# Kernel tuning notes

Hardware: AMD Instinct MI355X
Metric: run time of the kernel (lower is better)

The kernel has to match this reference:

```python
import jax, jax.numpy as jnp
import numpy as np

N_NODES = 100000
N_EDGES = 1600000
IN_FEATS = 128
N_HIDDEN = 32
N_CLASSES = 40
HEADS = (8, 8, 1)
NEG_SLOPE = 0.2  # PyG GATConv default leaky_relu slope


def gat_conv(h, src, dst, W, a_src, a_dst, b, n_nodes):
    """PyG-style GATConv (concat=True, eval mode, self-loops already added).
    h: [N, Fin], W: [Fin, H*C], a_src/a_dst: [H, C], b: [H*C].
    """
    H, C = a_src.shape
    x = (h @ W).reshape(n_nodes, H, C)                      # [N, H, C]
    al_src = jnp.sum(x * a_src[None], axis=-1)              # [N, H]
    al_dst = jnp.sum(x * a_dst[None], axis=-1)              # [N, H]
    e = jax.nn.leaky_relu(al_src[src] + al_dst[dst], NEG_SLOPE)  # [E, H]
    # numerically-stable softmax over each destination node's neighborhood
    m = jax.ops.segment_max(e, dst, num_segments=n_nodes)   # [N, H]
    w = jnp.exp(e - m[dst])                                 # [E, H]
    s = jax.ops.segment_sum(w, dst, num_segments=n_nodes)   # [N, H]
    alpha = w / s[dst]                                      # [E, H]
    out = jax.ops.segment_sum(x[src] * alpha[:, :, None], dst,
                              num_segments=n_nodes)         # [N, H, C]
    return out.reshape(n_nodes, H * C) + b


def _layer_params(key, fin, heads, cout):
    k1, k2, k3 = jax.random.split(key, 3)
    W = jax.random.normal(k1, (fin, heads * cout), dtype=jnp.float32) * (1.0 / np.sqrt(fin))
    a_src = jax.random.normal(k2, (heads, cout), dtype=jnp.float32) * 0.1
    a_dst = jax.random.normal(k3, (heads, cout), dtype=jnp.float32) * 0.1
    b = jnp.zeros((heads * cout,), dtype=jnp.float32)
    return W, a_src, a_dst, b


def setup_inputs() -> dict:
    key = jax.random.key(0)
    ks = jax.random.split(key, 5)
    features = jax.random.normal(ks[0], (N_NODES, IN_FEATS), dtype=jnp.float32)
    edge_index = jax.random.randint(ks[1], (2, N_EDGES), 0, N_NODES, dtype=jnp.int64)
    W0, a_src0, a_dst0, b0 = _layer_params(ks[2], IN_FEATS, HEADS[0], N_HIDDEN)
    W1, a_src1, a_dst1, b1 = _layer_params(ks[3], N_HIDDEN * HEADS[0], HEADS[1], N_HIDDEN)
    W2, a_src2, a_dst2, b2 = _layer_params(ks[4], N_HIDDEN * HEADS[1], HEADS[2], N_CLASSES)
    return {
        "features": features, "edge_index": edge_index,
        "W0": W0, "a_src0": a_src0, "a_dst0": a_dst0, "b0": b0,
        "W1": W1, "a_src1": a_src1, "a_dst1": a_dst1, "b1": b1,
        "W2": W2, "a_src2": a_src2, "a_dst2": a_dst2, "b2": b2,
    }


def reference(features, edge_index, W0, a_src0, a_dst0, b0,
              W1, a_src1, a_dst1, b1, W2, a_src2, a_dst2, b2):
    n = features.shape[0]
    loops = jnp.arange(n, dtype=edge_index.dtype)
    src = jnp.concatenate([edge_index[0], loops])  # add_self_loops=True (PyG default)
    dst = jnp.concatenate([edge_index[1], loops])
    # eval mode: F.dropout is identity
    h = gat_conv(features, src, dst, W0, a_src0, a_dst0, b0, n)
    h = jax.nn.elu(h)
    h = gat_conv(h, src, dst, W1, a_src1, a_dst1, b1, n)
    h = jax.nn.elu(h)
    h = gat_conv(h, src, dst, W2, a_src2, a_dst2, b2, n)
    return h
```

## Files before the change

### kernel.cpp

```cpp
#include <hip/hip_runtime.h>
#include <hip/hip_bf16.h>
#include <hip/hip_fp16.h>
#include <math.h>

typedef __attribute__((ext_vector_type(8))) short short8;
typedef __attribute__((ext_vector_type(8))) _Float16 half8;
typedef __attribute__((ext_vector_type(4))) float f32x4;
typedef unsigned short ushort_t;
typedef unsigned long long u64_t;
struct __align__(8) us4 { ushort_t x, y, z, w; };

__device__ __forceinline__ ushort_t f2bf(float f) {
    unsigned u = __float_as_uint(f);
    u += 0x7FFFu + ((u >> 16) & 1u);
    return (ushort_t)(u >> 16);
}
__device__ __forceinline__ float bf2f(ushort_t h) {
    return __uint_as_float(((unsigned)h) << 16);
}

__device__ __forceinline__ void store_out(float* p, float v) { *p = v; }
__device__ __forceinline__ void store_out(__half* p, float v) { *p = __float2half(v); }

__global__ void detect64_k(const int* __restrict__ ei, int n_check,
                           int* __restrict__ flag, int* __restrict__ gtot) {
    int t = threadIdx.x;
    gtot[t] = 0; gtot[t + 256] = 0;
    if (t < 64) {
        int zeros = 0;
        for (int i = t; i < n_check; i += 64) zeros += (ei[2 * i + 1] == 0) ? 1 : 0;
        #pragma unroll
        for (int off = 1; off < 64; off <<= 1) zeros += __shfl_xor(zeros, off);
        if (t == 0) *flag = (zeros >= n_check - 2) ? 1 : 0;
    }
}

__device__ __forceinline__ void edge_sd(const int* __restrict__ ei, int e, int E,
                                        int is64, int N, int& s_, int& d_) {
    if (e >= E) { s_ = d_ = e - E; return; }
    int s, d;
    if (is64) { s = ei[2 * e]; d = ei[2 * (E + e)]; }
    else      { s = ei[e];     d = ei[E + e]; }
    s_ = ((unsigned)s < (unsigned)N) ? s : 0;
    d_ = ((unsigned)d < (unsigned)N) ? d : 0;
}


__global__ __launch_bounds__(256) void csr_hist_k(
    const int* __restrict__ ei, const int* __restrict__ flag,
    int* __restrict__ gtot, int E, int Etot, int N) {
    __shared__ int hc[512];
    int t = threadIdx.x;
    hc[t] = 0; hc[t + 256] = 0;
    __syncthreads();
    int base = blockIdx.x * 4096;
    int is64 = *flag;
    for (int k = 0; k < 16; ++k) {
        int e = base + k * 256 + t;
        if (e < Etot) {
            int s_, d_;
            edge_sd(ei, e, E, is64, N, s_, d_);
            atomicAdd(&hc[d_ >> 8], 1);
        }
    }
    __syncthreads();
    if (hc[t])       atomicAdd(&gtot[t], hc[t]);
    if (hc[t + 256]) atomicAdd(&gtot[t + 256], hc[t + 256]);
}

__global__ void csr_scanb_k(const int* __restrict__ gtot, int* __restrict__ boff,
                            int* __restrict__ gcur, int B) {
    __shared__ int tmp[512];
    int t = threadIdx.x;
    int v = (t < B) ? gtot[t] : 0;
    tmp[t] = v;
    __syncthreads();
    for (int off = 1; off < 512; off <<= 1) {
        int x = (t >= off) ? tmp[t - off] : 0;
        __syncthreads();
        tmp[t] += x;
        __syncthreads();
    }
    if (t < B) {
        int excl = tmp[t] - v;
        boff[t] = excl;
        gcur[t] = excl;
    }
    if (t == B - 1) boff[B] = tmp[t];
}

__global__ __launch_bounds__(256) void csr_stage_k(
    const int* __restrict__ ei, const int* __restrict__ flag,
    int* __restrict__ gcur, u64_t* __restrict__ staging,
    int E, int Etot, int N) {
    __shared__ int bcnt[512];
    __shared__ int resv[512];
    int t = threadIdx.x;
    bcnt[t] = 0; bcnt[t + 256] = 0;
    __syncthreads();
    int base = blockIdx.x * 4096;
    int is64 = *flag;
    u64_t pk[16];
    #pragma unroll
    for (int k = 0; k < 16; ++k) {
        int e = base + k * 256 + t;
        pk[k] = ~0ull;
        if (e < Etot) {
            int s_, d_;
            edge_sd(ei, e, E, is64, N, s_, d_);
            pk[k] = ((u64_t)(unsigned)d_ << 32) | (unsigned)s_;
            atomicAdd(&bcnt[d_ >> 8], 1);
        }
    }
    __syncthreads();
    {
        int c0 = bcnt[t];
        resv[t] = c0 ? atomicAdd(&gcur[t], c0) : 0;
        int c1 = bcnt[t + 256];
        resv[t + 256] = c1 ? atomicAdd(&gcur[t + 256], c1) : 0;
    }
    __syncthreads();
    bcnt[t] = 0; bcnt[t + 256] = 0;
    __syncthreads();
    #pragma unroll
    for (int k = 0; k < 16; ++k) {
        if (pk[k] != ~0ull) {
            int b = (int)(pk[k] >> 40);
            int pos = resv[b] + atomicAdd(&bcnt[b], 1);
            staging[pos] = pk[k];
        }
    }
}

__global__ __launch_bounds__(256) void csr_fine_k(
    const u64_t* __restrict__ staging, const int* __restrict__ boff,
    int* __restrict__ rowptr, int* __restrict__ csr_src, int N, int Etot) {
    __shared__ int hcnt[256];
    __shared__ int scn[256];
    const int b = blockIdx.x, t = threadIdx.x;
    const int lo = b << 8;
    const int base = boff[b], cnt = boff[b + 1] - base;
    hcnt[t] = 0;
    __syncthreads();
    for (int i = t; i < cnt; i += 256) {
        int dst = (int)(staging[base + i] >> 32);
        atomicAdd(&hcnt[dst - lo], 1);
    }
    __syncthreads();
    int v = hcnt[t];
    scn[t] = v;
    __syncthreads();
    for (int off = 1; off < 256; off <<= 1) {
        int x = (t >= off) ? scn[t - off] : 0;
        __syncthreads();
        scn[t] += x;
        __syncthreads();
    }
    int excl = scn[t] - v;
    if (lo + t < N) rowptr[lo + t] = base + excl;
    hcnt[t] = base + excl;
    __syncthreads();
    for (int i = t; i < cnt; i += 256) {
        u64_t pd = staging[base + i];
        int dst = (int)(pd >> 32);
        int pos = atomicAdd(&hcnt[dst - lo], 1);
        csr_src[pos] = (int)(pd & 0xFFFFFFFFu);
    }
    if (b == 0 && t == 0) rowptr[N] = Etot;
}

__global__ void splitw_bf16_k(const float* __restrict__ W, ushort_t* __restrict__ Wh,
                              ushort_t* __restrict__ Wl, int K, int M, int Mp) {
    int i = blockIdx.x * 256 + threadIdx.x;
    if (i >= Mp * K) return;
    int n = i / K, k = i - n * K;
    float v = (n < M) ? W[(size_t)k * M + n] : 0.f;
    ushort_t h = f2bf(v);
    Wh[i] = h;
    Wl[i] = f2bf(v - bf2f(h));
}

__global__ void splitw_f16_k(const float* __restrict__ W, ushort_t* __restrict__ Wh,
                             ushort_t* __restrict__ Wl, int K, int M, int Mp) {
    int i = blockIdx.x * 256 + threadIdx.x;
    if (i >= Mp * K) return;
    int n = i / K, k = i - n * K;
    float v = (n < M) ? W[(size_t)k * M + n] : 0.f;
    __half h = __float2half(v);
    Wh[i] = __half_as_ushort(h);
    Wl[i] = __half_as_ushort(__float2half(v - __half2float(h)));
}

__global__ __launch_bounds__(256) void splitA_k(const float* __restrict__ A,
                                                ushort_t* __restrict__ Hh,
                                                ushort_t* __restrict__ Hl,
                                                long total4) {
    long i = ((long)blockIdx.x * 256 + threadIdx.x) * 4;
    if (i >= total4) return;
    float4 v = *(const float4*)&A[i];
    us4 h, l;
    h.x = f2bf(v.x); l.x = f2bf(v.x - bf2f(h.x));
    h.y = f2bf(v.y); l.y = f2bf(v.y - bf2f(h.y));
    h.z = f2bf(v.z); l.z = f2bf(v.z - bf2f(h.z));
    h.w = f2bf(v.w); l.w = f2bf(v.w - bf2f(h.w));
    *(us4*)&Hh[i] = h;
    *(us4*)&Hl[i] = l;
}

template <int BN, int WMCNT, int WNCNT, typename TOUT, int LMODE>
__global__ __launch_bounds__(256) void mfma_gemm_k(const ushort_t* __restrict__ Ahg,
                                                   const ushort_t* __restrict__ Alg,
                                                   const ushort_t* __restrict__ BhT,
                                                   const ushort_t* __restrict__ BlT,
                                                   TOUT* __restrict__ C,
                                                   int N, int K, int M,
                                                   const float* __restrict__ a_s,
                                                   const float* __restrict__ a_d,
                                                   float* __restrict__ alS,
                                                   float* __restrict__ alD) {
    constexpr int BM = 128;
    constexpr int PAD = 40;
    constexpr int WMX = BM / WMCNT;
    constexpr int WNX = BN / WNCNT;
    constexpr int FM = WMX / 16, FN = WNX / 16;
    static_assert(FN == 4, "logit epilogue assumes WNX==64");

    __shared__ ushort_t Ah[BM * PAD], Al[BM * PAD];
    __shared__ ushort_t Bh[BN * PAD], Bl[BN * PAD];

    const int tx = threadIdx.x;
    const int wave = tx >> 6, lane = tx & 63;
    const int quad = lane >> 4, l16 = lane & 15;
    const int br = blockIdx.y * BM, bc = blockIdx.x * BN;
    const int wm = (wave / WNCNT) * WMX;
    const int wn = (wave % WNCNT) * WNX;

    f32x4 acc[FM][FN] = {};

    for (int k0 = 0; k0 < K; k0 += 32) {
        #pragma unroll
        for (int r = 0; r < 2; ++r) {
            int i = r * 256 + tx;
            int m = i >> 2, k8 = (i & 3) * 8;
            int gr = br + m;
            short8 vh = {}, vl = {};
            if (gr < N) {
                vh = *(const short8*)&Ahg[(size_t)gr * K + k0 + k8];
                vl = *(const short8*)&Alg[(size_t)gr * K + k0 + k8];
            }
            *(short8*)&Ah[m * PAD + k8] = vh;
            *(short8*)&Al[m * PAD + k8] = vl;
        }
        #pragma unroll
        for (int r = 0; r < BN / 64; ++r) {
            int i = r * 256 + tx;
            int n = i >> 2, k8 = (i & 3) * 8;
            *(short8*)&Bh[n * PAD + k8] = *(const short8*)&BhT[(size_t)(bc + n) * K + k0 + k8];
            *(short8*)&Bl[n * PAD + k8] = *(const short8*)&BlT[(size_t)(bc + n) * K + k0 + k8];
        }
        __syncthreads();

        short8 afh[FM], afl[FM];
        #pragma unroll
        for (int mi = 0; mi < FM; ++mi) {
            int row = wm + mi * 16 + l16;
            afh[mi] = *(const short8*)&Ah[row * PAD + quad * 8];
            afl[mi] = *(const short8*)&Al[row * PAD + quad * 8];
        }
        #pragma unroll
        for (int ni = 0; ni < FN; ++ni) {
            int row = wn + ni * 16 + l16;
            short8 bfh = *(const short8*)&Bh[row * PAD + quad * 8];
            short8 bfl = *(const short8*)&Bl[row * PAD + quad * 8];
            #pragma unroll
            for (int mi = 0; mi < FM; ++mi) {
                acc[mi][ni] = __builtin_amdgcn_mfma_f32_16x16x32_bf16(afh[mi], bfh, acc[mi][ni], 0, 0, 0);
                acc[mi][ni] = __builtin_amdgcn_mfma_f32_16x16x32_bf16(afh[mi], bfl, acc[mi][ni], 0, 0, 0);
                acc[mi][ni] = __builtin_amdgcn_mfma_f32_16x16x32_bf16(afl[mi], bfh, acc[mi][ni], 0, 0, 0);
            }
        }
        __syncthreads();
    }

    #pragma unroll
    for (int mi = 0; mi < FM; ++mi) {
        #pragma unroll
        for (int ni = 0; ni < FN; ++ni) {
            int gc = bc + wn + ni * 16 + l16;
            if (gc >= M) continue;
            #pragma unroll
            for (int r = 0; r < 4; ++r) {
                int gr = br + wm + mi * 16 + quad * 4 + r;
                if (gr < N) store_out(&C[(size_t)gr * M + gc], acc[mi][ni][r]);
            }
        }
    }

    float aSv[FN], aDv[FN];
    #pragma unroll
    for (int ni = 0; ni < FN; ++ni) {
        int gc = bc + wn + ni * 16 + l16;
        bool ok = gc < M;
        aSv[ni] = ok ? a_s[gc] : 0.f;
        aDv[ni] = ok ? a_d[gc] : 0.f;
    }
    if (LMODE == 1) {
        #pragma unroll
        for (int mi = 0; mi < FM; ++mi) {
            #pragma unroll
            for (int r = 0; r < 4; ++r) {
                float p1a = acc[mi][0][r] * aSv[0] + acc[mi][1][r] * aSv[1];
                float p1b = acc[mi][2][r] * aSv[2] + acc[mi][3][r] * aSv[3];
                float p2a = acc[mi][0][r] * aDv[0] + acc[mi][1][r] * aDv[1];
                float p2b = acc[mi][2][r] * aDv[2] + acc[mi][3][r] * aDv[3];
                #pragma unroll
                for (int off = 1; off < 16; off <<= 1) {
                    p1a += __shfl_xor(p1a, off);
                    p1b += __shfl_xor(p1b, off);
                    p2a += __shfl_xor(p2a, off);
                    p2b += __shfl_xor(p2b, off);
                }
                if (l16 == 0) {
                    int gr = br + wm + mi * 16 + quad * 4 + r;
                    if (gr < N) {
                        int hb = (bc + wn) >> 5;
                        alS[gr * 8 + hb]     = p1a;
                        alS[gr * 8 + hb + 1] = p1b;
                        alD[gr * 8 + hb]     = p2a;
                        alD[gr * 8 + hb + 1] = p2b;
                    }
                }
            }
        }
    } else {
        #pragma unroll
        for (int mi = 0; mi < FM; ++mi) {
            #pragma unroll
            for (int r = 0; r < 4; ++r) {
                float p1 = acc[mi][0][r] * aSv[0] + acc[mi][1][r] * aSv[1]
                         + acc[mi][2][r] * aSv[2] + acc[mi][3][r] * aSv[3];
                float p2 = acc[mi][0][r] * aDv[0] + acc[mi][1][r] * aDv[1]
                         + acc[mi][2][r] * aDv[2] + acc[mi][3][r] * aDv[3];
                #pragma unroll
                for (int off = 1; off < 16; off <<= 1) {
                    p1 += __shfl_xor(p1, off);
                    p2 += __shfl_xor(p2, off);
                }
                if (l16 == 0) {
                    int gr = br + wm + mi * 16 + quad * 4 + r;
                    if (gr < N) { alS[gr] = p1; alD[gr] = p2; }
                }
            }
        }
    }
}

template <int BN, int WMCNT, int WNCNT, typename TOUT, int LMODE>
__global__ __launch_bounds__(256) void mfma_gemm_f16_k(const __half* __restrict__ A,
                                                       const ushort_t* __restrict__ BhT,
                                                       const ushort_t* __restrict__ BlT,
                                                       TOUT* __restrict__ C,
                                                       int N, int K, int M,
                                                       const float* __restrict__ a_s,
                                                       const float* __restrict__ a_d,
                                                       float* __restrict__ alS,
                                                       float* __restrict__ alD) {
    constexpr int BM = 128;
    constexpr int PAD = 40;
    constexpr int WMX = BM / WMCNT;
    constexpr int WNX = BN / WNCNT;
    constexpr int FM = WMX / 16, FN = WNX / 16;
    static_assert(FN == 4, "logit epilogue assumes WNX==64");

    __shared__ ushort_t Ah[BM * PAD];
    __shared__ ushort_t Bh[BN * PAD], Bl[BN * PAD];

    const int tx = threadIdx.x;
    const int wave = tx >> 6, lane = tx & 63;
    const int quad = lane >> 4, l16 = lane & 15;
    const int br = blockIdx.y * BM, bc = blockIdx.x * BN;
    const int wm = (wave / WNCNT) * WMX;
    const int wn = (wave % WNCNT) * WNX;

    f32x4 acc[FM][FN] = {};

    for (int k0 = 0; k0 < K; k0 += 32) {
        #pragma unroll
        for (int r = 0; r < 2; ++r) {
            int i = r * 256 + tx;
            int m = i >> 2, k8 = (i & 3) * 8;
            int gr = br + m;
            short8 v = {};
            if (gr < N) v = *(const short8*)&A[(size_t)gr * K + k0 + k8];
            *(short8*)&Ah[m * PAD + k8] = v;
        }
        #pragma unroll
        for (int r = 0; r < BN / 64; ++r) {
            int i = r * 256 + tx;
            int n = i >> 2, k8 = (i & 3) * 8;
            *(short8*)&Bh[n * PAD + k8] = *(const short8*)&BhT[(size_t)(bc + n) * K + k0 + k8];
            *(short8*)&Bl[n * PAD + k8] = *(const short8*)&BlT[(size_t)(bc + n) * K + k0 + k8];
        }
        __syncthreads();

        half8 af[FM];
        #pragma unroll
        for (int mi = 0; mi < FM; ++mi) {
            int row = wm + mi * 16 + l16;
            af[mi] = *(const half8*)&Ah[row * PAD + quad * 8];
        }
        #pragma unroll
        for (int ni = 0; ni < FN; ++ni) {
            int row = wn + ni * 16 + l16;
            half8 bfh = *(const half8*)&Bh[row * PAD + quad * 8];
            half8 bfl = *(const half8*)&Bl[row * PAD + quad * 8];
            #pragma unroll
            for (int mi = 0; mi < FM; ++mi) {
                acc[mi][ni] = __builtin_amdgcn_mfma_f32_16x16x32_f16(af[mi], bfh, acc[mi][ni], 0, 0, 0);
                acc[mi][ni] = __builtin_amdgcn_mfma_f32_16x16x32_f16(af[mi], bfl, acc[mi][ni], 0, 0, 0);
            }
        }
        __syncthreads();
    }

    #pragma unroll
    for (int mi = 0; mi < FM; ++mi) {
        #pragma unroll
        for (int ni = 0; ni < FN; ++ni) {
            int gc = bc + wn + ni * 16 + l16;
            if (gc >= M) continue;
            #pragma unroll
            for (int r = 0; r < 4; ++r) {
                int gr = br + wm + mi * 16 + quad * 4 + r;
                if (gr < N) store_out(&C[(size_t)gr * M + gc], acc[mi][ni][r]);
            }
        }
    }

    float aSv[FN], aDv[FN];
    #pragma unroll
    for (int ni = 0; ni < FN; ++ni) {
        int gc = bc + wn + ni * 16 + l16;
        bool ok = gc < M;
        aSv[ni] = ok ? a_s[gc] : 0.f;
        aDv[ni] = ok ? a_d[gc] : 0.f;
    }
    if (LMODE == 1) {
        #pragma unroll
        for (int mi = 0; mi < FM; ++mi) {
            #pragma unroll
            for (int r = 0; r < 4; ++r) {
                float p1a = acc[mi][0][r] * aSv[0] + acc[mi][1][r] * aSv[1];
                float p1b = acc[mi][2][r] * aSv[2] + acc[mi][3][r] * aSv[3];
                float p2a = acc[mi][0][r] * aDv[0] + acc[mi][1][r] * aDv[1];
                float p2b = acc[mi][2][r] * aDv[2] + acc[mi][3][r] * aDv[3];
                #pragma unroll
                for (int off = 1; off < 16; off <<= 1) {
                    p1a += __shfl_xor(p1a, off);
                    p1b += __shfl_xor(p1b, off);
                    p2a += __shfl_xor(p2a, off);
                    p2b += __shfl_xor(p2b, off);
                }
                if (l16 == 0) {
                    int gr = br + wm + mi * 16 + quad * 4 + r;
                    if (gr < N) {
                        int hb = (bc + wn) >> 5;
                        alS[gr * 8 + hb]     = p1a;
                        alS[gr * 8 + hb + 1] = p1b;
                        alD[gr * 8 + hb]     = p2a;
                        alD[gr * 8 + hb + 1] = p2b;
                    }
                }
            }
        }
    } else {
        #pragma unroll
        for (int mi = 0; mi < FM; ++mi) {
            #pragma unroll
            for (int r = 0; r < 4; ++r) {
                float p1 = acc[mi][0][r] * aSv[0] + acc[mi][1][r] * aSv[1]
                         + acc[mi][2][r] * aSv[2] + acc[mi][3][r] * aSv[3];
                float p2 = acc[mi][0][r] * aDv[0] + acc[mi][1][r] * aDv[1]
                         + acc[mi][2][r] * aDv[2] + acc[mi][3][r] * aDv[3];
                #pragma unroll
                for (int off = 1; off < 16; off <<= 1) {
                    p1 += __shfl_xor(p1, off);
                    p2 += __shfl_xor(p2, off);
                }
                if (l16 == 0) {
                    int gr = br + wm + mi * 16 + quad * 4 + r;
                    if (gr < N) { alS[gr] = p1; alD[gr] = p2; }
                }
            }
        }
    }
}

__global__ __launch_bounds__(256) void node_aggr8_k(
    const int* __restrict__ rowptr, const int* __restrict__ csr_src,
    const float* __restrict__ alS, const float* __restrict__ alD,
    const __half* __restrict__ xh, const float* __restrict__ bias,
    __half* __restrict__ out, int N, int do_elu) {
    __shared__ int    lsrc[4][64];
    __shared__ __half lalpha[4][64 * 8];
    const int wv = threadIdx.x >> 6;
    int wid = (blockIdx.x * 256 + threadIdx.x) >> 6;
    int lane = threadIdx.x & 63;
    if (wid >= N) return;
    const int d = wid;
    const int beg = rowptr[d], end = rowptr[d + 1];
    const int deg = end - beg;
    const int dcap = deg < 64 ? deg : 64;

    const int h = lane & 7, esub = lane >> 3;
    const float aDh = alD[d * 8 + h];

    const int nch = (deg + 7) >> 3;

    float exv[8] = {};
    float s = 0.f;
    #pragma unroll
    for (int c = 0; c < 8; ++c) {
        int sl = c * 8 + esub;
        int e = beg + sl;
        if (e < end) {
            int src = csr_src[e];
            float ev = alS[src * 8 + h] + aDh;
            ev = ev > 0.f ? ev : 0.2f * ev;
            float ex = __expf(fminf(ev, 30.f));
            if (h == 0) lsrc[wv][sl] = src;
            exv[c] = ex;
            s += ex;
        }
    }
    for (int c = 8; c < nch; ++c) {
        int e = beg + c * 8 + esub;
        if (e < end) {
            int src = csr_src[e];
            float ev = alS[src * 8 + h] + aDh;
            ev = ev > 0.f ? ev : 0.2f * ev;
            s += __expf(fminf(ev, 30.f));
        }
    }
    #pragma unroll
    for (int off = 8; off < 64; off <<= 1) s += __shfl_xor(s, off);

    float rsl = 1.f / s;
    #pragma unroll
    for (int c = 0; c < 8; ++c) {
        int sl = c * 8 + esub;
        if (sl < dcap) lalpha[wv][sl * 8 + h] = __float2half(exv[c] * rsl);
    }

    const int g = lane & 31;
    const int hh = g >> 2;
    const int p = lane >> 5;
    const float rs = __shfl(rsl, hh);

    const char* xb = (const char*)xh;
    const unsigned goff = (unsigned)(g << 4);

    const int T = (dcap + 1) >> 1;
    __half2 a2q[4];
    float4 rq[4];
    __half2 hacc[4] = {};

    #pragma unroll
    for (int i = 0; i < 4; ++i) {
        int e0 = 2 * i + p;
        int idx = e0 < dcap ? e0 : dcap - 1;
        int sv = lsrc[wv][idx];
        ushort_t ub = __half_as_ushort(lalpha[wv][idx * 8 + hh]);
        if (e0 >= dcap) ub = 0;
        a2q[i] = __half2half2(__ushort_as_half(ub));
        rq[i] = *(const float4*)(xb + (((unsigned)sv << 9) + goff));
    }

    #define PROC8(i)                                                        \
    {                                                                       \
        float4 raw = rq[i];                                                 \
        __half2 a2 = a2q[i];                                                \
        int e0 = 2 * (t + 4 + (i)) + p;                                     \
        ushort_t ub = 0;                                                    \
        if (e0 < dcap) {                                                    \
            int srcn = lsrc[wv][e0];                                        \
            ub = __half_as_ushort(lalpha[wv][e0 * 8 + hh]);                 \
            rq[i] = *(const float4*)(xb + (((unsigned)srcn << 9) + goff));  \
        }                                                                   \
        a2q[i] = __half2half2(__ushort_as_half(ub));                        \
        const __half2* hp = (const __half2*)&raw;                           \
        hacc[0] = __hfma2(hp[0], a2, hacc[0]);                              \
        hacc[1] = __hfma2(hp[1], a2, hacc[1]);                              \
        hacc[2] = __hfma2(hp[2], a2, hacc[2]);                              \
        hacc[3] = __hfma2(hp[3], a2, hacc[3]);                              \
    }
    #define TAIL8(i)                                                        \
    {                                                                       \
        float4 raw = rq[i];                                                 \
        __half2 a2 = a2q[i];                                                \
        const __half2* hp = (const __half2*)&raw;                           \
        hacc[0] = __hfma2(hp[0], a2, hacc[0]);                              \
        hacc[1] = __hfma2(hp[1], a2, hacc[1]);                              \
        hacc[2] = __hfma2(hp[2], a2, hacc[2]);                              \
        hacc[3] = __hfma2(hp[3], a2, hacc[3]);                              \
    }
    int t = 0;
    for (; t + 4 <= T; t += 4) { PROC8(0) PROC8(1) PROC8(2) PROC8(3) }
    {
        int rem = T - t;
        if (rem > 0) { TAIL8(0) if (rem > 1) { TAIL8(1) if (rem > 2) TAIL8(2) } }
    }
    #undef PROC8
    #undef TAIL8

    for (int c = 8; c < nch; ++c) {
        int base = beg + c * 8;
        int e = base + esub;
        int src_l = 0; float ex_l = 0.f;
        if (e < end) {
            src_l = csr_src[e];
            float ev = alS[src_l * 8 + h] + aDh;
            ev = ev > 0.f ? ev : 0.2f * ev;
            ex_l = __expf(fminf(ev, 30.f));
        }
        int cnt = end - base; if (cnt > 8) cnt = 8;
        int steps = (cnt + 1) >> 1;
        for (int t2 = 0; t2 < steps; ++t2) {
            int j = t2 * 2 + p;
            int jc = j < cnt ? j : (cnt - 1);
            int src = __shfl(src_l, jc * 8);
            float af = __shfl(ex_l, jc * 8 + hh) * rs;
            if (j >= cnt) af = 0.f;
            __half2 a2 = __float2half2_rn(af);
            const float4 raw = *(const float4*)(xb + (((unsigned)src << 9) + goff));
            const __half2* hp = (const __half2*)&raw;
            hacc[0] = __hfma2(hp[0], a2, hacc[0]);
            hacc[1] = __hfma2(hp[1], a2, hacc[1]);
            hacc[2] = __hfma2(hp[2], a2, hacc[2]);
            hacc[3] = __hfma2(hp[3], a2, hacc[3]);
        }
    }

    #pragma unroll
    for (int k = 0; k < 4; ++k) {
        int vi = __shfl_xor(*(int*)&hacc[k], 32);
        hacc[k] = __hadd2(hacc[k], *(__half2*)&vi);
    }

    if (p == 0) {
        float2 f0 = __half22float2(hacc[0]);
        float2 f1 = __half22float2(hacc[1]);
        float2 f2 = __half22float2(hacc[2]);
        float2 f3 = __half22float2(hacc[3]);
        const float4 bv0 = *(const float4*)&bias[g * 8];
        const float4 bv1 = *(const float4*)&bias[g * 8 + 4];
        float o[8];
        o[0] = f0.x + bv0.x; o[1] = f0.y + bv0.y;
        o[2] = f1.x + bv0.z; o[3] = f1.y + bv0.w;
        o[4] = f2.x + bv1.x; o[5] = f2.y + bv1.y;
        o[6] = f3.x + bv1.z; o[7] = f3.y + bv1.w;
        if (do_elu) {
            #pragma unroll
            for (int k = 0; k < 8; ++k) o[k] = o[k] > 0.f ? o[k] : (__expf(o[k]) - 1.f);
        }
        float4 st;
        ((__half2*)&st)[0] = __floats2half2_rn(o[0], o[1]);
        ((__half2*)&st)[1] = __floats2half2_rn(o[2], o[3]);
        ((__half2*)&st)[2] = __floats2half2_rn(o[4], o[5]);
        ((__half2*)&st)[3] = __floats2half2_rn(o[6], o[7]);
        *(float4*)(out + ((size_t)d << 8) + g * 8) = st;
    }
}

__global__ __launch_bounds__(256) void node_aggr1_k(
    const int* __restrict__ rowptr, const int* __restrict__ csr_src,
    const float* __restrict__ alS, const float* __restrict__ alD,
    const __half* __restrict__ xh2, const float* __restrict__ bias,
    float* __restrict__ out, int N) {
    __shared__ int   lsrc1[4][64];
    __shared__ float lal1[4][64];
    const int wv = threadIdx.x >> 6;
    int wid = (blockIdx.x * 256 + threadIdx.x) >> 6;
    int lane = threadIdx.x & 63;
    if (wid >= N) return;
    const int d = wid;
    const int beg = rowptr[d], end = rowptr[d + 1];
    const int deg = end - beg;
    const int dcap = deg < 64 ? deg : 64;
    const float aD = alD[d];

    float ex0 = 0.f;
    {
        int e = beg + lane;
        if (e < end) {
            int src0 = csr_src[e];
            float ev = alS[src0] + aD;
            ev = ev > 0.f ? ev : 0.2f * ev;
            ex0 = __expf(fminf(ev, 30.f));
            lsrc1[wv][lane] = src0;
        }
    }
    float s = ex0;
    for (int e = beg + 64 + lane; e < end; e += 64) {
        int src = csr_src[e];
        float ev = alS[src] + aD;
        ev = ev > 0.f ? ev : 0.2f * ev;
        s += __expf(fminf(ev, 30.f));
    }
    #pragma unroll
    for (int off = 1; off < 64; off <<= 1) s += __shfl_xor(s, off);
    const float rs = 1.f / s;
    if (lane < dcap) lal1[wv][lane] = ex0 * rs;

    const int q = lane & 31;
    const int p = lane >> 5;
    const int qg = q < 20 ? q : 19;
    const unsigned qb = (unsigned)(qg << 2);
    const char* xb2 = (const char*)xh2;

    const int T = (dcap + 1) >> 1;
    float alq[4];
    __half2 rq1[4];
    float ax = 0.f, ay = 0.f;

    #pragma unroll
    for (int i = 0; i < 4; ++i) {
        int e0 = 2 * i + p;
        int idx = e0 < dcap ? e0 : dcap - 1;
        int sv = lsrc1[wv][idx];
        float av = lal1[wv][idx];
        alq[i] = e0 < dcap ? av : 0.f;
        rq1[i] = *(const __half2*)(xb2 + ((unsigned)sv * 80u + qb));
    }

    #define PROC1(i)                                                        \
    {                                                                       \
        float2 rf = __half22float2(rq1[i]);                                 \
        float al = alq[i];                                                  \
        int e0 = 2 * (t + 4 + (i)) + p;                                     \
        float an = 0.f;                                                     \
        if (e0 < dcap) {                                                    \
            int sv = lsrc1[wv][e0];                                         \
            an = lal1[wv][e0];                                              \
            rq1[i] = *(const __half2*)(xb2 + ((unsigned)sv * 80u + qb));    \
        }                                                                   \
        alq[i] = an;                                                        \
        ax += rf.x * al; ay += rf.y * al;                                   \
    }
    #define TAIL1(i)                                                        \
    {                                                                       \
        float2 rf = __half22float2(rq1[i]);                                 \
        ax += rf.x * alq[i]; ay += rf.y * alq[i];                           \
    }
    int t = 0;
    for (; t + 4 <= T; t += 4) { PROC1(0) PROC1(1) PROC1(2) PROC1(3) }
    {
        int rem = T - t;
        if (rem > 0) { TAIL1(0) if (rem > 1) { TAIL1(1) if (rem > 2) TAIL1(2) } }
    }
    #undef PROC1
    #undef TAIL1

    for (int eb = beg + 64; eb < end; eb += 64) {
        int e = eb + lane;
        int cnt = end - eb; if (cnt > 64) cnt = 64;
        if (e < end) {
            int srcl = csr_src[e];
            float ev = alS[srcl] + aD;
            ev = ev > 0.f ? ev : 0.2f * ev;
            lsrc1[wv][lane] = srcl;
            lal1[wv][lane] = __expf(fminf(ev, 30.f)) * rs;
        }
        int T2 = (cnt + 1) >> 1;
        for (int t2 = 0; t2 < T2; ++t2) {
            int e0 = 2 * t2 + p;
            float al = 0.f;
            int sv = lsrc1[wv][0];
            if (e0 < cnt) { sv = lsrc1[wv][e0]; al = lal1[wv][e0]; }
            float2 rf = __half22float2(*(const __half2*)(xb2 + ((unsigned)sv * 80u + qb)));
            ax += rf.x * al; ay += rf.y * al;
        }
    }

    ax += __shfl_xor(ax, 32);
    ay += __shfl_xor(ay, 32);

    if (p == 0 && q < 20) {
        float2 bv = *(const float2*)&bias[q * 2];
        float2 st = make_float2(ax + bv.x, ay + bv.y);
        *(float2*)&out[(size_t)d * 40 + q * 2] = st;
    }
}

extern "C" void kernel_launch(void* const* d_in, const int* in_sizes, int n_in,
                              void* d_out, int out_size, void* d_ws, size_t ws_size,
                              hipStream_t stream) {
    const float* feat = (const float*)d_in[0];
    const int*   ei   = (const int*)d_in[1];
    const float* W0   = (const float*)d_in[2];
    const float* a0s  = (const float*)d_in[3];
    const float* a0d  = (const float*)d_in[4];
    const float* b0   = (const float*)d_in[5];
    const float* W1   = (const float*)d_in[6];
    const float* a1s  = (const float*)d_in[7];
    const float* a1d  = (const float*)d_in[8];
    const float* b1   = (const float*)d_in[9];
    const float* W2   = (const float*)d_in[10];
    const float* a2s  = (const float*)d_in[11];
    const float* a2d  = (const float*)d_in[12];
    const float* b2   = (const float*)d_in[13];
    float* out = (float*)d_out;

    const int N = in_sizes[0] / 128;
    const int E = in_sizes[1] / 2;
    const int Etot = E + N;

    __half* hbuf = (__half*)d_ws;
    __half* xh   = hbuf + (size_t)N * 256;
    __half* x2h  = xh + (size_t)N * 256;
    float*  alS  = (float*)(x2h + (size_t)N * 40);
    float*  alD  = alS + (size_t)N * 8;
    int* rowptr   = (int*)(alD + (size_t)N * 8);
    int* gtot     = rowptr + N + 1;
    int* boff     = gtot + 512;
    int* gcur     = boff + 513;
    int* csr_src  = gcur + 512;
    int* flag     = csr_src + Etot;
    uintptr_t wsp = ((uintptr_t)(flag + 1) + 15) & ~(uintptr_t)15;
    ushort_t* w0h = (ushort_t*)wsp;
    ushort_t* w0l = w0h + 256 * 128;
    ushort_t* w1h = w0l + 256 * 128;
    ushort_t* w1l = w1h + 256 * 256;
    ushort_t* w2h = w1l + 256 * 256;
    ushort_t* w2l = w2h + 64 * 256;

    u64_t* staging = (u64_t*)xh;

    ushort_t* fh = (ushort_t*)hbuf;
    ushort_t* fl = fh + (size_t)N * 128;

    const int B     = (N + 255) >> 8;
    const int nb_e4 = (Etot + 4095) / 4096;
    const int nb_nw = (N + 3) / 4;

    detect64_k<<<1, 256, 0, stream>>>(ei, 512, flag, gtot);
    csr_hist_k<<<nb_e4, 256, 0, stream>>>(ei, flag, gtot, E, Etot, N);
    csr_scanb_k<<<1, 512, 0, stream>>>(gtot, boff, gcur, B);
    csr_stage_k<<<nb_e4, 256, 0, stream>>>(ei, flag, gcur, staging, E, Etot, N);
    csr_fine_k<<<B, 256, 0, stream>>>(staging, boff, rowptr, csr_src, N, Etot);
    splitw_bf16_k<<<128, 256, 0, stream>>>(W0, w0h, w0l, 128, 256, 256);
    splitw_f16_k<<<256, 256, 0, stream>>>(W1, w1h, w1l, 256, 256, 256);
    splitw_f16_k<<<64, 256, 0, stream>>>(W2, w2h, w2l, 256, 40, 64);
    splitA_k<<<(int)(((long)N * 128 / 4 + 255) / 256), 256, 0, stream>>>(
        feat, fh, fl, (long)N * 128);

    const int mb = (N + 127) / 128;

    mfma_gemm_k<128, 2, 2, __half, 1><<<dim3(2, mb), 256, 0, stream>>>(
        fh, fl, w0h, w0l, xh, N, 128, 256, a0s, a0d, alS, alD);
    node_aggr8_k<<<nb_nw, 256, 0, stream>>>(rowptr, csr_src, alS, alD, xh, b0,
                                            hbuf, N, 1);

    mfma_gemm_f16_k<128, 2, 2, __half, 1><<<dim3(2, mb), 256, 0, stream>>>(
        hbuf, w1h, w1l, xh, N, 256, 256, a1s, a1d, alS, alD);
    node_aggr8_k<<<nb_nw, 256, 0, stream>>>(rowptr, csr_src, alS, alD, xh, b1,
                                            hbuf, N, 1);

    mfma_gemm_f16_k<64, 4, 1, __half, 2><<<dim3(1, mb), 256, 0, stream>>>(
        hbuf, w2h, w2l, x2h, N, 256, 40, a2s, a2d, alS, alD);
    node_aggr1_k<<<nb_nw, 256, 0, stream>>>(rowptr, csr_src, alS, alD, x2h, b2,
                                            out, N);
}
```

Before: 665.3 us.

## Use direct global-to-LDS loads in GEMMs, fuse prep kernels, pad layer-3 rows

The GEMM tile loads now use global_load_lds, which writes straight into unpadded shared memory and skips the register staging. Out-of-range rows are clamped to the last row rather than zero-filled. The four weight and feature split kernels are merged into one launch to cut launch overhead. The layer-3 projection is stored with a padded 64-column stride so the final aggregation can read 8-byte chunks, with 16 lanes per edge and 4 edges in flight per wave. Dropping the LDS padding may bring back bank conflicts on the fragment reads.

```diff
diff --git a/kernel.cpp b/kernel.cpp
--- a/kernel.cpp
+++ b/kernel.cpp
@@ -9,6 +9,11 @@
 typedef unsigned short ushort_t;
 typedef unsigned long long u64_t;
 struct __align__(8) us4 { ushort_t x, y, z, w; };
+
+#define GLDS16(gsrc, ldst)                                                   \
+    __builtin_amdgcn_global_load_lds(                                        \
+        (const __attribute__((address_space(1))) void*)(gsrc),               \
+        (__attribute__((address_space(3))) void*)(ldst), 16, 0, 0)
 
 __device__ __forceinline__ ushort_t f2bf(float f) {
     unsigned u = __float_as_uint(f);
@@ -44,7 +49,6 @@
     s_ = ((unsigned)s < (unsigned)N) ? s : 0;
     d_ = ((unsigned)d < (unsigned)N) ? d : 0;
 }
-
 
 __global__ __launch_bounds__(256) void csr_hist_k(
     const int* __restrict__ ei, const int* __restrict__ flag,
@@ -169,42 +173,47 @@
     if (b == 0 && t == 0) rowptr[N] = Etot;
 }
 
-__global__ void splitw_bf16_k(const float* __restrict__ W, ushort_t* __restrict__ Wh,
-                              ushort_t* __restrict__ Wl, int K, int M, int Mp) {
-    int i = blockIdx.x * 256 + threadIdx.x;
-    if (i >= Mp * K) return;
-    int n = i / K, k = i - n * K;
-    float v = (n < M) ? W[(size_t)k * M + n] : 0.f;
-    ushort_t h = f2bf(v);
-    Wh[i] = h;
-    Wl[i] = f2bf(v - bf2f(h));
-}
-
-__global__ void splitw_f16_k(const float* __restrict__ W, ushort_t* __restrict__ Wh,
-                             ushort_t* __restrict__ Wl, int K, int M, int Mp) {
-    int i = blockIdx.x * 256 + threadIdx.x;
-    if (i >= Mp * K) return;
-    int n = i / K, k = i - n * K;
-    float v = (n < M) ? W[(size_t)k * M + n] : 0.f;
-    __half h = __float2half(v);
-    Wh[i] = __half_as_ushort(h);
-    Wl[i] = __half_as_ushort(__float2half(v - __half2float(h)));
-}
-
-__global__ __launch_bounds__(256) void splitA_k(const float* __restrict__ A,
-                                                ushort_t* __restrict__ Hh,
-                                                ushort_t* __restrict__ Hl,
-                                                long total4) {
-    long i = ((long)blockIdx.x * 256 + threadIdx.x) * 4;
-    if (i >= total4) return;
-    float4 v = *(const float4*)&A[i];
-    us4 h, l;
-    h.x = f2bf(v.x); l.x = f2bf(v.x - bf2f(h.x));
-    h.y = f2bf(v.y); l.y = f2bf(v.y - bf2f(h.y));
-    h.z = f2bf(v.z); l.z = f2bf(v.z - bf2f(h.z));
-    h.w = f2bf(v.w); l.w = f2bf(v.w - bf2f(h.w));
-    *(us4*)&Hh[i] = h;
-    *(us4*)&Hl[i] = l;
+__global__ __launch_bounds__(256) void prep_k(
+    const float* __restrict__ W0, const float* __restrict__ W1,
+    const float* __restrict__ W2, const float* __restrict__ feat,
+    ushort_t* __restrict__ w0h, ushort_t* __restrict__ w0l,
+    ushort_t* __restrict__ w1h, ushort_t* __restrict__ w1l,
+    ushort_t* __restrict__ w2h, ushort_t* __restrict__ w2l,
+    ushort_t* __restrict__ fh, ushort_t* __restrict__ fl, long totalA4) {
+    int b = blockIdx.x, tx = threadIdx.x;
+    if (b < 128) {
+        int i = b * 256 + tx;
+        int n = i >> 7, k = i & 127;
+        float v = W0[(size_t)k * 256 + n];
+        ushort_t h = f2bf(v);
+        w0h[i] = h;
+        w0l[i] = f2bf(v - bf2f(h));
+    } else if (b < 384) {
+        int i = (b - 128) * 256 + tx;
+        int n = i >> 8, k = i & 255;
+        float v = W1[(size_t)k * 256 + n];
+        __half h = __float2half(v);
+        w1h[i] = __half_as_ushort(h);
+        w1l[i] = __half_as_ushort(__float2half(v - __half2float(h)));
+    } else if (b < 448) {
+        int i = (b - 384) * 256 + tx;
+        int n = i >> 8, k = i & 255;
+        float v = (n < 40) ? W2[(size_t)k * 40 + n] : 0.f;
+        __half h = __float2half(v);
+        w2h[i] = __half_as_ushort(h);
+        w2l[i] = __half_as_ushort(__float2half(v - __half2float(h)));
+    } else {
+        long i = ((long)(b - 448) * 256 + tx) * 4;
+        if (i >= totalA4) return;
+        float4 v = *(const float4*)&feat[i];
+        us4 h, l;
+        h.x = f2bf(v.x); l.x = f2bf(v.x - bf2f(h.x));
+        h.y = f2bf(v.y); l.y = f2bf(v.y - bf2f(h.y));
+        h.z = f2bf(v.z); l.z = f2bf(v.z - bf2f(h.z));
+        h.w = f2bf(v.w); l.w = f2bf(v.w - bf2f(h.w));
+        *(us4*)&fh[i] = h;
+        *(us4*)&fl[i] = l;
+    }
 }
 
 template <int BN, int WMCNT, int WNCNT, typename TOUT, int LMODE>
@@ -213,20 +222,19 @@
                                                    const ushort_t* __restrict__ BhT,
                                                    const ushort_t* __restrict__ BlT,
                                                    TOUT* __restrict__ C,
-                                                   int N, int K, int M,
+                                                   int N, int K, int M, int Mst,
                                                    const float* __restrict__ a_s,
                                                    const float* __restrict__ a_d,
                                                    float* __restrict__ alS,
                                                    float* __restrict__ alD) {
     constexpr int BM = 128;
-    constexpr int PAD = 40;
     constexpr int WMX = BM / WMCNT;
     constexpr int WNX = BN / WNCNT;
     constexpr int FM = WMX / 16, FN = WNX / 16;
     static_assert(FN == 4, "logit epilogue assumes WNX==64");
 
-    __shared__ ushort_t Ah[BM * PAD], Al[BM * PAD];
-    __shared__ ushort_t Bh[BN * PAD], Bl[BN * PAD];
+    __shared__ ushort_t Ah[BM * 32], Al[BM * 32];
+    __shared__ ushort_t Bh[BN * 32], Bl[BN * 32];
 
     const int tx = threadIdx.x;
     const int wave = tx >> 6, lane = tx & 63;
@@ -241,22 +249,19 @@
         #pragma unroll
         for (int r = 0; r < 2; ++r) {
             int i = r * 256 + tx;
-            int m = i >> 2, k8 = (i & 3) * 8;
-            int gr = br + m;
-            short8 vh = {}, vl = {};
-            if (gr < N) {
-                vh = *(const short8*)&Ahg[(size_t)gr * K + k0 + k8];
-                vl = *(const short8*)&Alg[(size_t)gr * K + k0 + k8];
-            }
-            *(short8*)&Ah[m * PAD + k8] = vh;
-            *(short8*)&Al[m * PAD + k8] = vl;
+            int m = i >> 2, kc = (i & 3) * 8;
+            int gr = br + m; gr = gr < N ? gr : N - 1;
+            size_t go = (size_t)gr * K + k0 + kc;
+            GLDS16(&Ahg[go], &Ah[(size_t)i * 8]);
+            GLDS16(&Alg[go], &Al[(size_t)i * 8]);
         }
         #pragma unroll
         for (int r = 0; r < BN / 64; ++r) {
             int i = r * 256 + tx;
-            int n = i >> 2, k8 = (i & 3) * 8;
-            *(short8*)&Bh[n * PAD + k8] = *(const short8*)&BhT[(size_t)(bc + n) * K + k0 + k8];
-            *(short8*)&Bl[n * PAD + k8] = *(const short8*)&BlT[(size_t)(bc + n) * K + k0 + k8];
+            int n = i >> 2, kc = (i & 3) * 8;
+            size_t go = (size_t)(bc + n) * K + k0 + kc;
+            GLDS16(&BhT[go], &Bh[(size_t)i * 8]);
+            GLDS16(&BlT[go], &Bl[(size_t)i * 8]);
         }
         __syncthreads();
 
@@ -264,14 +269,14 @@
         #pragma unroll
         for (int mi = 0; mi < FM; ++mi) {
             int row = wm + mi * 16 + l16;
-            afh[mi] = *(const short8*)&Ah[row * PAD + quad * 8];
-            afl[mi] = *(const short8*)&Al[row * PAD + quad * 8];
+            afh[mi] = *(const short8*)&Ah[row * 32 + quad * 8];
+            afl[mi] = *(const short8*)&Al[row * 32 + quad * 8];
         }
         #pragma unroll
         for (int ni = 0; ni < FN; ++ni) {
             int row = wn + ni * 16 + l16;
-            short8 bfh = *(const short8*)&Bh[row * PAD + quad * 8];
-            short8 bfl = *(const short8*)&Bl[row * PAD + quad * 8];
+            short8 bfh = *(const short8*)&Bh[row * 32 + quad * 8];
+            short8 bfl = *(const short8*)&Bl[row * 32 + quad * 8];
             #pragma unroll
             for (int mi = 0; mi < FM; ++mi) {
                 acc[mi][ni] = __builtin_amdgcn_mfma_f32_16x16x32_bf16(afh[mi], bfh, acc[mi][ni], 0, 0, 0);
@@ -287,11 +292,10 @@
         #pragma unroll
         for (int ni = 0; ni < FN; ++ni) {
             int gc = bc + wn + ni * 16 + l16;
-            if (gc >= M) continue;
             #pragma unroll
             for (int r = 0; r < 4; ++r) {
                 int gr = br + wm + mi * 16 + quad * 4 + r;
-                if (gr < N) store_out(&C[(size_t)gr * M + gc], acc[mi][ni][r]);
+                if (gr < N) store_out(&C[(size_t)gr * Mst + gc], acc[mi][ni][r]);
             }
         }
     }
@@ -360,20 +364,19 @@
                                                        const ushort_t* __restrict__ BhT,
                                                        const ushort_t* __restrict__ BlT,
                                                        TOUT* __restrict__ C,
-                                                       int N, int K, int M,
+                                                       int N, int K, int M, int Mst,
                                                        const float* __restrict__ a_s,
                                                        const float* __restrict__ a_d,
                                                        float* __restrict__ alS,
                                                        float* __restrict__ alD) {
     constexpr int BM = 128;
-    constexpr int PAD = 40;
     constexpr int WMX = BM / WMCNT;
     constexpr int WNX = BN / WNCNT;
     constexpr int FM = WMX / 16, FN = WNX / 16;
     static_assert(FN == 4, "logit epilogue assumes WNX==64");
 
-    __shared__ ushort_t Ah[BM * PAD];
-    __shared__ ushort_t Bh[BN * PAD], Bl[BN * PAD];
+    __shared__ ushort_t Ah[BM * 32];
+    __shared__ ushort_t Bh[BN * 32], Bl[BN * 32];
 
     const int tx = threadIdx.x;
     const int wave = tx >> 6, lane = tx & 63;
@@ -388,18 +391,17 @@
         #pragma unroll
         for (int r = 0; r < 2; ++r) {
             int i = r * 256 + tx;
-            int m = i >> 2, k8 = (i & 3) * 8;
-            int gr = br + m;
-            short8 v = {};
-            if (gr < N) v = *(const short8*)&A[(size_t)gr * K + k0 + k8];
-            *(short8*)&Ah[m * PAD + k8] = v;
+            int m = i >> 2, kc = (i & 3) * 8;
+            int gr = br + m; gr = gr < N ? gr : N - 1;
+            GLDS16(&A[(size_t)gr * K + k0 + kc], &Ah[(size_t)i * 8]);
         }
         #pragma unroll
         for (int r = 0; r < BN / 64; ++r) {
             int i = r * 256 + tx;
-            int n = i >> 2, k8 = (i & 3) * 8;
-            *(short8*)&Bh[n * PAD + k8] = *(const short8*)&BhT[(size_t)(bc + n) * K + k0 + k8];
-            *(short8*)&Bl[n * PAD + k8] = *(const short8*)&BlT[(size_t)(bc + n) * K + k0 + k8];
+            int n = i >> 2, kc = (i & 3) * 8;
+            size_t go = (size_t)(bc + n) * K + k0 + kc;
+            GLDS16(&BhT[go], &Bh[(size_t)i * 8]);
+            GLDS16(&BlT[go], &Bl[(size_t)i * 8]);
         }
         __syncthreads();
 
@@ -407,13 +409,13 @@
         #pragma unroll
         for (int mi = 0; mi < FM; ++mi) {
             int row = wm + mi * 16 + l16;
-            af[mi] = *(const half8*)&Ah[row * PAD + quad * 8];
+            af[mi] = *(const half8*)&Ah[row * 32 + quad * 8];
         }
         #pragma unroll
         for (int ni = 0; ni < FN; ++ni) {
             int row = wn + ni * 16 + l16;
-            half8 bfh = *(const half8*)&Bh[row * PAD + quad * 8];
-            half8 bfl = *(const half8*)&Bl[row * PAD + quad * 8];
+            half8 bfh = *(const half8*)&Bh[row * 32 + quad * 8];
+            half8 bfl = *(const half8*)&Bl[row * 32 + quad * 8];
             #pragma unroll
             for (int mi = 0; mi < FM; ++mi) {
                 acc[mi][ni] = __builtin_amdgcn_mfma_f32_16x16x32_f16(af[mi], bfh, acc[mi][ni], 0, 0, 0);
@@ -428,11 +430,10 @@
         #pragma unroll
         for (int ni = 0; ni < FN; ++ni) {
             int gc = bc + wn + ni * 16 + l16;
-            if (gc >= M) continue;
             #pragma unroll
             for (int r = 0; r < 4; ++r) {
                 int gr = br + wm + mi * 16 + quad * 4 + r;
-                if (gr < N) store_out(&C[(size_t)gr * M + gc], acc[mi][ni][r]);
+                if (gr < N) store_out(&C[(size_t)gr * Mst + gc], acc[mi][ni][r]);
             }
         }
     }
@@ -712,45 +713,51 @@
     const float rs = 1.f / s;
     if (lane < dcap) lal1[wv][lane] = ex0 * rs;
 
-    const int q = lane & 31;
-    const int p = lane >> 5;
-    const int qg = q < 20 ? q : 19;
-    const unsigned qb = (unsigned)(qg << 2);
+    const int p = lane >> 4;
+    const int q = lane & 15;
+    const unsigned qb = (unsigned)(q << 3);
     const char* xb2 = (const char*)xh2;
 
-    const int T = (dcap + 1) >> 1;
+    const int T = (dcap + 3) >> 2;
     float alq[4];
-    __half2 rq1[4];
-    float ax = 0.f, ay = 0.f;
+    float2 rq1[4];
+    float a0 = 0.f, a1 = 0.f, a2 = 0.f, a3 = 0.f;
 
     #pragma unroll
     for (int i = 0; i < 4; ++i) {
-        int e0 = 2 * i + p;
+        int e0 = 4 * i + p;
         int idx = e0 < dcap ? e0 : dcap - 1;
         int sv = lsrc1[wv][idx];
         float av = lal1[wv][idx];
         alq[i] = e0 < dcap ? av : 0.f;
-        rq1[i] = *(const __half2*)(xb2 + ((unsigned)sv * 80u + qb));
+        rq1[i] = *(const float2*)(xb2 + (((unsigned)sv << 7) + qb));
     }
 
     #define PROC1(i)                                                        \
     {                                                                       \
-        float2 rf = __half22float2(rq1[i]);                                 \
+        float2 raw = rq1[i];                                                \
         float al = alq[i];                                                  \
-        int e0 = 2 * (t + 4 + (i)) + p;                                     \
+        int e0 = 4 * (t + 4 + (i)) + p;                                     \
         float an = 0.f;                                                     \
         if (e0 < dcap) {                                                    \
             int sv = lsrc1[wv][e0];                                         \
             an = lal1[wv][e0];                                              \
-            rq1[i] = *(const __half2*)(xb2 + ((unsigned)sv * 80u + qb));    \
+            rq1[i] = *(const float2*)(xb2 + (((unsigned)sv << 7) + qb));    \
         }                                                                   \
         alq[i] = an;                                                        \
-        ax += rf.x * al; ay += rf.y * al;                                   \
+        float2 lo = __half22float2(((const __half2*)&raw)[0]);              \
+        float2 hi = __half22float2(((const __half2*)&raw)[1]);              \
+        a0 += lo.x * al; a1 += lo.y * al;                                   \
+        a2 += hi.x * al; a3 += hi.y * al;                                   \
     }
     #define TAIL1(i)                                                        \
     {                                                                       \
-        float2 rf = __half22float2(rq1[i]);                                 \
-        ax += rf.x * alq[i]; ay += rf.y * alq[i];                           \
+        float2 raw = rq1[i];                                                \
+        float al = alq[i];                                                  \
+        float2 lo = __half22float2(((const __half2*)&raw)[0]);              \
+        float2 hi = __half22float2(((const __half2*)&raw)[1]);              \
+        a0 += lo.x * al; a1 += lo.y * al;                                   \
+        a2 += hi.x * al; a3 += hi.y * al;                                   \
     }
     int t = 0;
     for (; t + 4 <= T; t += 4) { PROC1(0) PROC1(1) PROC1(2) PROC1(3) }
@@ -771,24 +778,29 @@
             lsrc1[wv][lane] = srcl;
             lal1[wv][lane] = __expf(fminf(ev, 30.f)) * rs;
         }
-        int T2 = (cnt + 1) >> 1;
+        int T2 = (cnt + 3) >> 2;
         for (int t2 = 0; t2 < T2; ++t2) {
-            int e0 = 2 * t2 + p;
+            int e0 = 4 * t2 + p;
             float al = 0.f;
             int sv = lsrc1[wv][0];
             if (e0 < cnt) { sv = lsrc1[wv][e0]; al = lal1[wv][e0]; }
-            float2 rf = __half22float2(*(const __half2*)(xb2 + ((unsigned)sv * 80u + qb)));
-            ax += rf.x * al; ay += rf.y * al;
-        }
-    }
-
-    ax += __shfl_xor(ax, 32);
-    ay += __shfl_xor(ay, 32);
-
-    if (p == 0 && q < 20) {
-        float2 bv = *(const float2*)&bias[q * 2];
-        float2 st = make_float2(ax + bv.x, ay + bv.y);
-        *(float2*)&out[(size_t)d * 40 + q * 2] = st;
+            float2 raw = *(const float2*)(xb2 + (((unsigned)sv << 7) + qb));
+            float2 lo = __half22float2(((const __half2*)&raw)[0]);
+            float2 hi = __half22float2(((const __half2*)&raw)[1]);
+            a0 += lo.x * al; a1 += lo.y * al;
+            a2 += hi.x * al; a3 += hi.y * al;
+        }
+    }
+
+    a0 += __shfl_xor(a0, 16); a0 += __shfl_xor(a0, 32);
+    a1 += __shfl_xor(a1, 16); a1 += __shfl_xor(a1, 32);
+    a2 += __shfl_xor(a2, 16); a2 += __shfl_xor(a2, 32);
+    a3 += __shfl_xor(a3, 16); a3 += __shfl_xor(a3, 32);
+
+    if (p == 0 && q < 10) {
+        const float4 bv = *(const float4*)&bias[q * 4];
+        float4 st = make_float4(a0 + bv.x, a1 + bv.y, a2 + bv.z, a3 + bv.w);
+        *(float4*)&out[(size_t)d * 40 + q * 4] = st;
     }
 }
 
@@ -818,7 +830,7 @@
     __half* hbuf = (__half*)d_ws;
     __half* xh   = hbuf + (size_t)N * 256;
     __half* x2h  = xh + (size_t)N * 256;
-    float*  alS  = (float*)(x2h + (size_t)N * 40);
+    float*  alS  = (float*)(x2h + (size_t)N * 64);
     float*  alD  = alS + (size_t)N * 8;
     int* rowptr   = (int*)(alD + (size_t)N * 8);
     int* gtot     = rowptr + N + 1;
@@ -848,26 +860,28 @@
     csr_scanb_k<<<1, 512, 0, stream>>>(gtot, boff, gcur, B);
     csr_stage_k<<<nb_e4, 256, 0, stream>>>(ei, flag, gcur, staging, E, Etot, N);
     csr_fine_k<<<B, 256, 0, stream>>>(staging, boff, rowptr, csr_src, N, Etot);
-    splitw_bf16_k<<<128, 256, 0, stream>>>(W0, w0h, w0l, 128, 256, 256);
-    splitw_f16_k<<<256, 256, 0, stream>>>(W1, w1h, w1l, 256, 256, 256);
-    splitw_f16_k<<<64, 256, 0, stream>>>(W2, w2h, w2l, 256, 40, 64);
-    splitA_k<<<(int)(((long)N * 128 / 4 + 255) / 256), 256, 0, stream>>>(
-        feat, fh, fl, (long)N * 128);
+    {
+        long totalA4 = (long)N * 128;
+        int nbA = (int)((totalA4 / 4 + 255) / 256);
+        prep_k<<<448 + nbA, 256, 0, stream>>>(W0, W1, W2, feat,
+                                              w0h, w0l, w1h, w1l, w2h, w2l,
+                                              fh, fl, totalA4);
+    }
 
     const int mb = (N + 127) / 128;
 
     mfma_gemm_k<128, 2, 2, __half, 1><<<dim3(2, mb), 256, 0, stream>>>(
-        fh, fl, w0h, w0l, xh, N, 128, 256, a0s, a0d, alS, alD);
+        fh, fl, w0h, w0l, xh, N, 128, 256, 256, a0s, a0d, alS, alD);
     node_aggr8_k<<<nb_nw, 256, 0, stream>>>(rowptr, csr_src, alS, alD, xh, b0,
                                             hbuf, N, 1);
 
     mfma_gemm_f16_k<128, 2, 2, __half, 1><<<dim3(2, mb), 256, 0, stream>>>(
-        hbuf, w1h, w1l, xh, N, 256, 256, a1s, a1d, alS, alD);
+        hbuf, w1h, w1l, xh, N, 256, 256, 256, a1s, a1d, alS, alD);
     node_aggr8_k<<<nb_nw, 256, 0, stream>>>(rowptr, csr_src, alS, alD, xh, b1,
                                             hbuf, N, 1);
 
     mfma_gemm_f16_k<64, 4, 1, __half, 2><<<dim3(1, mb), 256, 0, stream>>>(
-        hbuf, w2h, w2l, x2h, N, 256, 40, a2s, a2d, alS, alD);
+        hbuf, w2h, w2l, x2h, N, 256, 40, 64, a2s, a2d, alS, alD);
     node_aggr1_k<<<nb_nw, 256, 0, stream>>>(rowptr, csr_src, alS, alD, x2h, b2,
                                             out, N);
 }
```

New measurement: 655.8 us. Within noise of the previous version (-1.4%).
